# Performance work log

Hardware: AMD Instinct MI355X
Metric: run time of the kernel (lower is better)

Reference implementation:

```python
import jax, jax.numpy as jnp
import numpy as np


def _lstm_last(x, w_ih, w_hh, b_ih, b_hh):
    # x: [M, T, D] -> last hidden state [M, H]; PyTorch gate order i,f,g,o
    M = x.shape[0]
    H = w_hh.shape[1]
    xi = jnp.einsum('mtd,gd->tmg', x, w_ih) + b_ih + b_hh  # [T, M, 4H]
    def step(carry, xt):
        h, c = carry
        gates = xt + h @ w_hh.T
        i, f, g, o = jnp.split(gates, 4, axis=-1)
        c = jax.nn.sigmoid(f) * c + jax.nn.sigmoid(i) * jnp.tanh(g)
        h = jax.nn.sigmoid(o) * jnp.tanh(c)
        return (h, c), None
    z = jnp.zeros((M, H), x.dtype)
    (h, _), _ = jax.lax.scan(step, (z, z), xi)
    return h


def _gcn_conv(x, edge_index, w, b):
    # Symmetric-normalized GCN conv with self loops (PyG GCNConv defaults).
    # x: [BT, N, F] -> [BT, N, Hg]
    N = x.shape[1]
    loops = jnp.arange(N, dtype=edge_index.dtype)
    src = jnp.concatenate([edge_index[0], loops])
    dst = jnp.concatenate([edge_index[1], loops])
    deg = jnp.zeros((N,), x.dtype).at[dst].add(jnp.ones((), x.dtype))
    dinv = jax.lax.rsqrt(deg)  # deg >= 1 thanks to self loops
    norm = (dinv[src] * dinv[dst])[:, None]  # [E+N, 1]
    xw = x @ w                               # [BT, N, Hg]
    msg = xw[:, src, :] * norm               # gather along node axis
    out = jnp.zeros_like(xw).at[:, dst, :].add(msg)  # scatter-add
    return out + b


def setup_inputs() -> dict:
    key = jax.random.key(0)
    ks = jax.random.split(key, 16)
    B, T, N, F = 2, 12, 10000, 16
    Hg, H, P, E = 32, 64, 4, 160000
    sc = 0.1
    return {
        'era5_seq': jax.random.normal(ks[0], (B, T, N, F), jnp.float32),
        'zeta_seq': jax.random.normal(ks[1], (B, T, N), jnp.float32),
        'edge_index': jax.random.randint(ks[2], (2, E), 0, N, jnp.int32),
        'gcn_w': jax.random.normal(ks[3], (F, Hg), jnp.float32) * sc,
        'gcn_b': jnp.zeros((Hg,), jnp.float32),
        'w_ih1': jax.random.normal(ks[4], (4 * H, Hg), jnp.float32) * sc,
        'w_hh1': jax.random.normal(ks[5], (4 * H, H), jnp.float32) * sc,
        'b_ih1': jax.random.normal(ks[6], (4 * H,), jnp.float32) * sc,
        'b_hh1': jax.random.normal(ks[7], (4 * H,), jnp.float32) * sc,
        'w_ih2': jax.random.normal(ks[8], (4 * H, 1), jnp.float32) * sc,
        'w_hh2': jax.random.normal(ks[9], (4 * H, H), jnp.float32) * sc,
        'b_ih2': jax.random.normal(ks[10], (4 * H,), jnp.float32) * sc,
        'b_hh2': jax.random.normal(ks[11], (4 * H,), jnp.float32) * sc,
        'fc_w': jax.random.normal(ks[12], (P, 2 * H), jnp.float32) * sc,
        'fc_b': jnp.zeros((P,), jnp.float32),
    }


def reference(era5_seq, zeta_seq, edge_index, gcn_w, gcn_b, w_ih1, w_hh1, b_ih1, b_hh1, w_ih2, w_hh2, b_ih2, b_hh2, fc_w, fc_b):
    B, T, N, F = era5_seq.shape
    Hg = gcn_w.shape[1]
    # GCN over all (b, t) slices at once (replaces nested python loops)
    h = _gcn_conv(era5_seq.reshape(B * T, N, F), edge_index, gcn_w, gcn_b)
    gcn_seq = h.reshape(B, T, N, Hg).transpose(0, 2, 1, 3).reshape(B * N, T, Hg)
    spatial_feat = _lstm_last(gcn_seq, w_ih1, w_hh1, b_ih1, b_hh1)  # [B*N, H]
    z_seq = zeta_seq.transpose(0, 2, 1).reshape(B * N, T, 1)
    zeta_feat = _lstm_last(z_seq, w_ih2, w_hh2, b_ih2, b_hh2)        # [B*N, H]
    combined = jnp.concatenate([spatial_feat, zeta_feat], axis=-1)
    y = combined @ fc_w.T + fc_b                                     # [B*N, P]
    return y.reshape(B, N, -1).transpose(0, 2, 1)                    # [B, P, N]
```

## Files before the change

kernel.cpp:

```cpp
#include <hip/hip_runtime.h>
#include <hip/hip_bf16.h>
#include <stdint.h>

#define NN 10000
#define EE 160000
#define BB 2
#define TT 12
#define FF 16
#define HG 32
#define HH 64
#define PP 4
#define BT (BB*TT)
#define MM (BB*NN)
#define CAP 96
#define L2E 1.4426950408889634f

typedef _Float16 half8 __attribute__((ext_vector_type(8)));
typedef _Float16 h2 __attribute__((ext_vector_type(2)));
typedef float f32x4 __attribute__((ext_vector_type(4)));

union UP { uint32_t u; h2 h; };
union H8U { uint32_t u[4]; half8 v; };

__device__ __forceinline__ float sigm2(float a) {
  return __builtin_amdgcn_rcpf(1.0f + __builtin_amdgcn_exp2f(-a));
}
__device__ __forceinline__ float tanh2(float a) {
  return fmaf(-2.0f, __builtin_amdgcn_rcpf(1.0f + __builtin_amdgcn_exp2f(a)), 1.0f);
}
__device__ __forceinline__ float tanh2g(float a) {
  return fmaf(-2.0f * (2.0f * L2E),
              __builtin_amdgcn_rcpf(1.0f + __builtin_amdgcn_exp2f(a)),
              2.0f * L2E);
}

__device__ __forceinline__ void barrier_lds() {
  asm volatile("s_waitcnt lgkmcnt(0)" ::: "memory");
  __builtin_amdgcn_s_barrier();
  asm volatile("" ::: "memory");
}

#define FILL_BLKS (EE / 256)
#define PREP_BLKS ((NN * BT * 8) / 256)
__global__ __launch_bounds__(256) void k_prepfill(
    const int* __restrict__ eidx, int* __restrict__ cnt, int* __restrict__ csr,
    const float* __restrict__ era5, uint32_t* __restrict__ xt,
    const float* __restrict__ gcn_w,
    const float* __restrict__ w_ih1, const float* __restrict__ w_hh1,
    const float* __restrict__ b_ih1, const float* __restrict__ b_hh1,
    const float* __restrict__ w_ih2, const float* __restrict__ w_hh2,
    const float* __restrict__ b_ih2, const float* __restrict__ b_hh2,
    uint32_t* __restrict__ wbuf) {
  const int bid = blockIdx.x;
  const int tid = threadIdx.x;
  if (bid < FILL_BLKS) {
    int e = bid * 256 + tid;
    int d = eidx[EE + e];
    int pos = atomicAdd(&cnt[d], 1);
    if (pos < CAP) csr[d * CAP + pos] = eidx[e];
    return;
  }
  if (bid < FILL_BLKS + PREP_BLKS) {
    int D = (bid - FILL_BLKS) * 256 + tid;
    int f2 = D & 7;
    int bt = (D >> 3) % BT;
    int n = D / (8 * BT);
    const float* src = era5 + ((size_t)bt * NN + n) * FF + f2 * 2;
    UP u; u.h[0] = (_Float16)src[0]; u.h[1] = (_Float16)src[1];
    xt[D] = u.u;
    return;
  }
  const int wave = tid >> 6;
  const int lane = tid & 63;
  const int col = lane & 15;
  const int quad = lane >> 4;
#pragma unroll
  for (int g = 0; g < 4; ++g) {
    const float sc = (g == 2) ? 2.0f * L2E : L2E;
    int ncol = 16 * (wave + 4 * g) + col;
    wbuf[(0 + g) * 256 + tid] = __float_as_uint((b_ih1[ncol] + b_hh1[ncol]) * sc);
    wbuf[(4 + g) * 256 + tid] = __float_as_uint((b_ih2[ncol] + b_hh2[ncol]) * sc);
    wbuf[(8 + g) * 256 + tid] = __float_as_uint(w_ih2[ncol] * sc);
    H8U bx;
#pragma unroll
    for (int j = 0; j < 8; ++j)
      bx.v[j] = (_Float16)(w_ih1[ncol * HG + quad * 8 + j] * sc);
#pragma unroll
    for (int d = 0; d < 4; ++d) wbuf[(12 + g * 4 + d) * 256 + tid] = bx.u[d];
#pragma unroll
    for (int c2 = 0; c2 < 2; ++c2) {
      H8U b1, b2;
#pragma unroll
      for (int j = 0; j < 8; ++j) {
        b1.v[j] = (_Float16)(w_hh1[ncol * HH + c2 * 32 + quad * 8 + j] * sc);
        b2.v[j] = (_Float16)(w_hh2[ncol * HH + c2 * 32 + quad * 8 + j] * sc);
      }
#pragma unroll
      for (int d = 0; d < 4; ++d) {
        wbuf[(28 + (g * 2 + c2) * 4 + d) * 256 + tid] = b1.u[d];
        wbuf[(60 + (g * 2 + c2) * 4 + d) * 256 + tid] = b2.u[d];
      }
    }
  }
#pragma unroll
  for (int nt = 0; nt < 2; ++nt) {
#pragma unroll
    for (int d = 0; d < 4; ++d) {
      int k0 = quad * 8 + d * 2;
      int c = nt * 16 + col;
      UP u;
      u.h[0] = (k0 < FF)     ? (_Float16)gcn_w[k0 * HG + c]       : (_Float16)0.f;
      u.h[1] = (k0 + 1 < FF) ? (_Float16)gcn_w[(k0 + 1) * HG + c] : (_Float16)0.f;
      wbuf[(92 + nt * 4 + d) * 256 + tid] = u.u;
    }
  }
}

__global__ __launch_bounds__(256) void k_gather(const uint32_t* __restrict__ xt,
                                                const int* __restrict__ csr,
                                                const int* __restrict__ cnt,
                                                const float* __restrict__ gb,
                                                const uint32_t* __restrict__ wbuf,
                                                _Float16* __restrict__ gout) {
  __shared__ __align__(16) _Float16 aggh[4][32][40];
  const int tid = threadIdx.x;
  const int dloc = tid >> 6, lane = tid & 63;
  const int col = lane & 15, quad = lane >> 4;

  uint32_t* az = (uint32_t*)&aggh[dloc][0][0];
#pragma unroll
  for (int i = 0; i < 10; ++i) az[lane + 64 * i] = 0u;

  H8U Bg[2];
#pragma unroll
  for (int nt = 0; nt < 2; ++nt)
#pragma unroll
    for (int d = 0; d < 4; ++d) Bg[nt].u[d] = wbuf[(92 + nt * 4 + d) * 256 + tid];
  const float b0 = gb[col], b1 = gb[16 + col];

  const int dst = blockIdx.x * 4 + dloc;
  const int cdst = min(cnt[dst], CAP);
  const float dinv_d = rsqrtf((float)cdst + 1.0f);

  float acc[6];
#pragma unroll
  for (int i = 0; i < 6; ++i) acc[i] = 0.f;

  for (int base = 0; base < cdst; base += 64) {
    int mine = base + lane;
    int sv = dst; float dvv = 0.f;
    if (mine < cdst) {
      sv = csr[dst * CAP + mine];
      dvv = rsqrtf((float)cnt[sv] + 1.0f);
    }
    const int lim = min(64, cdst - base);
    for (int j = 0; j < lim; j += 4) {
      int sj[4]; float dj[4];
#pragma unroll
      for (int u = 0; u < 4; ++u) {
        int idx = j + u;
        sj[u] = __shfl(sv, idx);
        float d = __shfl(dvv, idx);
        dj[u] = (idx < lim) ? d : 0.f;
      }
      uint32_t dw[4][3];
#pragma unroll
      for (int u = 0; u < 4; ++u) {
        const uint32_t* row = xt + (size_t)sj[u] * 192;
#pragma unroll
        for (int k = 0; k < 3; ++k) dw[u][k] = row[lane + 64 * k];
      }
#pragma unroll
      for (int u = 0; u < 4; ++u) {
#pragma unroll
        for (int k = 0; k < 3; ++k) {
          UP up; up.u = dw[u][k];
          acc[2 * k]     = fmaf((float)up.h[0], dj[u], acc[2 * k]);
          acc[2 * k + 1] = fmaf((float)up.h[1], dj[u], acc[2 * k + 1]);
        }
      }
    }
  }
  const uint32_t* srow = xt + (size_t)dst * 192;
#pragma unroll
  for (int k = 0; k < 3; ++k) {
    UP u; u.u = srow[lane + 64 * k];
    int d0 = lane + 64 * k;
    int bt = d0 >> 3, f = (d0 & 7) * 2;
    UP o;
    o.h[0] = (_Float16)((acc[2 * k]     + (float)u.h[0] * dinv_d) * dinv_d);
    o.h[1] = (_Float16)((acc[2 * k + 1] + (float)u.h[1] * dinv_d) * dinv_d);
    *(uint32_t*)&aggh[dloc][bt][f] = o.u;
  }
  f32x4 C[2][2];
#pragma unroll
  for (int mt = 0; mt < 2; ++mt) {
    const half8 Af = *(const half8*)&aggh[dloc][mt * 16 + col][quad * 8];
#pragma unroll
    for (int nt = 0; nt < 2; ++nt) {
      float bb = nt ? b1 : b0;
      f32x4 ci; ci[0] = bb; ci[1] = bb; ci[2] = bb; ci[3] = bb;
      C[mt][nt] = __builtin_amdgcn_mfma_f32_16x16x32_f16(Af, Bg[nt].v, ci, 0, 0, 0);
    }
  }
#pragma unroll
  for (int mt = 0; mt < 2; ++mt)
#pragma unroll
    for (int r = 0; r < 4; ++r) {
      int bt = mt * 16 + quad * 4 + r;
      if (bt < BT) {
        int bb = (bt >= TT) ? 1 : 0;
        int t = bt - bb * TT;
#pragma unroll
        for (int nt = 0; nt < 2; ++nt) {
          int c = nt * 16 + col;
          gout[((size_t)(bb * NN + dst)) * 384 + t * 32 + c] = (_Float16)C[mt][nt][r];
        }
      }
    }
}

__global__ __launch_bounds__(256) void k_lstmfc(
    const _Float16* __restrict__ gout, const float* __restrict__ zeta,
    const uint32_t* __restrict__ wbuf,
    const float* __restrict__ fc_w, const float* __restrict__ fc_b,
    float* __restrict__ out) {
  const int m0 = blockIdx.x * 16;
  const int b = (m0 >= NN) ? 1 : 0;
  const int n0 = m0 - b * NN;
  const int tid = threadIdx.x;
  const int wave = tid >> 6;
  const int lane = tid & 63;
  const int col = lane & 15;
  const int quad = lane >> 4;

  float bias1[4], bias2[4], wx[4];
  H8U Bx[4], Bh1[4][2], Bh2[4][2];
#pragma unroll
  for (int g = 0; g < 4; ++g) {
    bias1[g] = __uint_as_float(wbuf[(0 + g) * 256 + tid]);
    bias2[g] = __uint_as_float(wbuf[(4 + g) * 256 + tid]);
    wx[g]    = __uint_as_float(wbuf[(8 + g) * 256 + tid]);
#pragma unroll
    for (int d = 0; d < 4; ++d) Bx[g].u[d] = wbuf[(12 + g * 4 + d) * 256 + tid];
#pragma unroll
    for (int c2 = 0; c2 < 2; ++c2)
#pragma unroll
      for (int d = 0; d < 4; ++d) {
        Bh1[g][c2].u[d] = wbuf[(28 + (g * 2 + c2) * 4 + d) * 256 + tid];
        Bh2[g][c2].u[d] = wbuf[(60 + (g * 2 + c2) * 4 + d) * 256 + tid];
      }
  }
  f32x4 bv1[4];
#pragma unroll
  for (int g = 0; g < 4; ++g) {
    f32x4 v = {bias1[g], bias1[g], bias1[g], bias1[g]};
    bv1[g] = v;
  }

  __shared__ union {
    struct {
      __align__(16) _Float16 hb1[2][16 * 72];
      __align__(16) _Float16 hb2[2][16 * 72];
    } h;
    float fcb[16][132];
  } su;
  __shared__ float zbuf[TT][16];

  if (tid < TT * 16) {
    int t = tid >> 4, s = tid & 15;
    zbuf[t][s] = zeta[((size_t)b * TT + t) * NN + n0 + s];
  }

  const _Float16* gbase = gout + (size_t)(m0 + col) * (TT * HG) + quad * 8;
  half8 A0 = *(const half8*)(gbase);

  float c1[4] = {0.f, 0.f, 0.f, 0.f}, c2v[4] = {0.f, 0.f, 0.f, 0.f};
  float h1f[4], h2f[4];

  barrier_lds();

#pragma unroll
  for (int t = 0; t < TT; ++t) {
    const int p = t & 1;
    if (t > 0) {
#pragma unroll
      for (int r = 0; r < 4; ++r) {
        int a = (quad * 4 + r) * 72 + 16 * wave + col;
        su.h.hb1[p][a] = (_Float16)h1f[r];
        su.h.hb2[p][a] = (_Float16)h2f[r];
      }
    }
    f32x4 a1[4], a2[4];
    const f32x4 z4 = *(const f32x4*)(&zbuf[t][quad * 4]);
#pragma unroll
    for (int g = 0; g < 4; ++g) {
      a1[g] = __builtin_amdgcn_mfma_f32_16x16x32_f16(A0, Bx[g].v, bv1[g], 0, 0, 0);
#pragma unroll
      for (int r = 0; r < 4; ++r)
        a2[g][r] = fmaf(wx[g], z4[r], bias2[g]);
    }
    if (t < TT - 1) A0 = *(const half8*)(gbase + (t + 1) * HG);
    if (t > 0) {
      barrier_lds();
      const half8 A11 = *(const half8*)(&su.h.hb1[p][col * 72 + quad * 8]);
      const half8 A21 = *(const half8*)(&su.h.hb1[p][col * 72 + 32 + quad * 8]);
      const half8 A12 = *(const half8*)(&su.h.hb2[p][col * 72 + quad * 8]);
      const half8 A22 = *(const half8*)(&su.h.hb2[p][col * 72 + 32 + quad * 8]);
#pragma unroll
      for (int g = 0; g < 4; ++g) {
        a1[g] = __builtin_amdgcn_mfma_f32_16x16x32_f16(A11, Bh1[g][0].v, a1[g], 0, 0, 0);
        a1[g] = __builtin_amdgcn_mfma_f32_16x16x32_f16(A21, Bh1[g][1].v, a1[g], 0, 0, 0);
        a2[g] = __builtin_amdgcn_mfma_f32_16x16x32_f16(A12, Bh2[g][0].v, a2[g], 0, 0, 0);
        a2[g] = __builtin_amdgcn_mfma_f32_16x16x32_f16(A22, Bh2[g][1].v, a2[g], 0, 0, 0);
      }
    }
#pragma unroll
    for (int r = 0; r < 4; ++r) {
      float i1 = sigm2(a1[0][r]), f1 = sigm2(a1[1][r]);
      float g1 = tanh2g(a1[2][r]), o1 = sigm2(a1[3][r]);
      c1[r] = fmaf(f1, c1[r], i1 * g1);
      h1f[r] = o1 * tanh2(c1[r]);
      float i2 = sigm2(a2[0][r]), f2 = sigm2(a2[1][r]);
      float g2 = tanh2g(a2[2][r]), o2 = sigm2(a2[3][r]);
      c2v[r] = fmaf(f2, c2v[r], i2 * g2);
      h2f[r] = o2 * tanh2(c2v[r]);
    }
  }
  barrier_lds();
#pragma unroll
  for (int r = 0; r < 4; ++r) {
    su.fcb[quad * 4 + r][16 * wave + col] = h1f[r];
    su.fcb[quad * 4 + r][64 + 16 * wave + col] = h2f[r];
  }
  barrier_lds();
  if (tid < 64) {
    int pp = tid >> 4, s = tid & 15;
    const f32x4* wr = (const f32x4*)(fc_w + pp * 128);
    const float* hv = su.fcb[s];
    float acc = fc_b[pp];
#pragma unroll
    for (int k = 0; k < 32; ++k) {
      f32x4 w4 = wr[k];
      acc += w4[0] * hv[4 * k] + w4[1] * hv[4 * k + 1] +
             w4[2] * hv[4 * k + 2] + w4[3] * hv[4 * k + 3];
    }
    out[((size_t)(b * PP + pp)) * NN + n0 + s] = acc;
  }
}

extern "C" void kernel_launch(void* const* d_in, const int* in_sizes, int n_in,
                              void* d_out, int out_size, void* d_ws, size_t ws_size,
                              hipStream_t stream) {
  (void)in_sizes; (void)n_in; (void)out_size; (void)ws_size;
  const float* era5  = (const float*)d_in[0];
  const float* zeta  = (const float*)d_in[1];
  const int*   eidx  = (const int*)d_in[2];
  const float* gcn_w = (const float*)d_in[3];
  const float* gcn_b = (const float*)d_in[4];
  const float* w_ih1 = (const float*)d_in[5];
  const float* w_hh1 = (const float*)d_in[6];
  const float* b_ih1 = (const float*)d_in[7];
  const float* b_hh1 = (const float*)d_in[8];
  const float* w_ih2 = (const float*)d_in[9];
  const float* w_hh2 = (const float*)d_in[10];
  const float* b_ih2 = (const float*)d_in[11];
  const float* b_hh2 = (const float*)d_in[12];
  const float* fc_w  = (const float*)d_in[13];
  const float* fc_b  = (const float*)d_in[14];
  float* out = (float*)d_out;

  char* ws = (char*)d_ws;
  int*      cnt  = (int*)(ws);
  int*      csr  = (int*)(ws + (64 << 10));
  uint32_t* xt   = (uint32_t*)(ws + (4ull << 20));
  uint32_t* gout = (uint32_t*)(ws + (12ull << 20));
  uint32_t* wbuf = (uint32_t*)(ws + (28ull << 20));

  hipMemsetAsync(cnt, 0, NN * sizeof(int), stream);
  k_prepfill<<<FILL_BLKS + PREP_BLKS + 1, 256, 0, stream>>>(
      eidx, cnt, csr, era5, xt, gcn_w,
      w_ih1, w_hh1, b_ih1, b_hh1, w_ih2, w_hh2, b_ih2, b_hh2, wbuf);
  k_gather<<<NN / 4, 256, 0, stream>>>(xt, csr, cnt, gcn_b, wbuf,
                                       (_Float16*)gout);
  k_lstmfc<<<MM / 16, 256, 0, stream>>>((const _Float16*)gout, zeta, wbuf,
                                        fc_w, fc_b, out);
}
```

Baseline: 176.7 us.

## Slice GCN gather over time chunks and double LSTM rows per block

The prep stage now lays out the fp16 node features as three slices of 8 (batch,time) pairs per node, and the gather kernel launches three times as many blocks, each aggregating one slice with one dword per lane. The aim is to shrink each block's working set for L2 locality and raise parallelism in the gather. The LSTM kernel now runs 512 threads on 32 rows per block, two independent 16-row groups with separate shared buffers, to amortise weight loads and barriers. The cost is that the edge list and degree lookups are re-read once per slice, and the larger blocks raise register and LDS pressure.

```diff
diff --git a/kernel.cpp b/kernel.cpp
--- a/kernel.cpp
+++ b/kernel.cpp
@@ -14,6 +14,8 @@
 #define MM (BB*NN)
 #define CAP 96
 #define L2E 1.4426950408889634f
+#define SL 3
+#define SBT 8
 
 typedef _Float16 half8 __attribute__((ext_vector_type(8)));
 typedef _Float16 h2 __attribute__((ext_vector_type(2)));
@@ -62,10 +64,13 @@
   }
   if (bid < FILL_BLKS + PREP_BLKS) {
     int D = (bid - FILL_BLKS) * 256 + tid;
-    int f2 = D & 7;
-    int bt = (D >> 3) % BT;
-    int n = D / (8 * BT);
-    const float* src = era5 + ((size_t)bt * NN + n) * FF + f2 * 2;
+    int s = D / (NN * 64);
+    int rem = D - s * (NN * 64);
+    int n = rem >> 6;
+    int l = rem & 63;
+    int btl = l >> 3, fp = l & 7;
+    int bt = s * SBT + btl;
+    const float* src = era5 + ((size_t)bt * NN + n) * FF + fp * 2;
     UP u; u.h[0] = (_Float16)src[0]; u.h[1] = (_Float16)src[1];
     xt[D] = u.u;
     return;
@@ -122,14 +127,16 @@
                                                 const float* __restrict__ gb,
                                                 const uint32_t* __restrict__ wbuf,
                                                 _Float16* __restrict__ gout) {
-  __shared__ __align__(16) _Float16 aggh[4][32][40];
+  __shared__ __align__(16) _Float16 aggh[4][16][40];
   const int tid = threadIdx.x;
   const int dloc = tid >> 6, lane = tid & 63;
   const int col = lane & 15, quad = lane >> 4;
+  const int s = blockIdx.x / (NN / 4);
+  const int b2 = blockIdx.x - s * (NN / 4);
 
   uint32_t* az = (uint32_t*)&aggh[dloc][0][0];
 #pragma unroll
-  for (int i = 0; i < 10; ++i) az[lane + 64 * i] = 0u;
+  for (int i = 0; i < 5; ++i) az[lane + 64 * i] = 0u;
 
   H8U Bg[2];
 #pragma unroll
@@ -138,14 +145,12 @@
     for (int d = 0; d < 4; ++d) Bg[nt].u[d] = wbuf[(92 + nt * 4 + d) * 256 + tid];
   const float b0 = gb[col], b1 = gb[16 + col];
 
-  const int dst = blockIdx.x * 4 + dloc;
+  const int dst = b2 * 4 + dloc;
   const int cdst = min(cnt[dst], CAP);
   const float dinv_d = rsqrtf((float)cdst + 1.0f);
-
-  float acc[6];
-#pragma unroll
-  for (int i = 0; i < 6; ++i) acc[i] = 0.f;
-
+  const uint32_t* xs = xt + (size_t)s * NN * 64;
+
+  float a0 = 0.f, a1v = 0.f;
   for (int base = 0; base < cdst; base += 64) {
     int mine = base + lane;
     int sv = dst; float dvv = 0.f;
@@ -154,101 +159,84 @@
       dvv = rsqrtf((float)cnt[sv] + 1.0f);
     }
     const int lim = min(64, cdst - base);
-    for (int j = 0; j < lim; j += 4) {
-      int sj[4]; float dj[4];
-#pragma unroll
-      for (int u = 0; u < 4; ++u) {
+    for (int j = 0; j < lim; j += 8) {
+      int sj[8]; float dj[8];
+#pragma unroll
+      for (int u = 0; u < 8; ++u) {
         int idx = j + u;
         sj[u] = __shfl(sv, idx);
         float d = __shfl(dvv, idx);
         dj[u] = (idx < lim) ? d : 0.f;
       }
-      uint32_t dw[4][3];
-#pragma unroll
-      for (int u = 0; u < 4; ++u) {
-        const uint32_t* row = xt + (size_t)sj[u] * 192;
-#pragma unroll
-        for (int k = 0; k < 3; ++k) dw[u][k] = row[lane + 64 * k];
-      }
-#pragma unroll
-      for (int u = 0; u < 4; ++u) {
-#pragma unroll
-        for (int k = 0; k < 3; ++k) {
-          UP up; up.u = dw[u][k];
-          acc[2 * k]     = fmaf((float)up.h[0], dj[u], acc[2 * k]);
-          acc[2 * k + 1] = fmaf((float)up.h[1], dj[u], acc[2 * k + 1]);
-        }
-      }
-    }
-  }
-  const uint32_t* srow = xt + (size_t)dst * 192;
-#pragma unroll
-  for (int k = 0; k < 3; ++k) {
-    UP u; u.u = srow[lane + 64 * k];
-    int d0 = lane + 64 * k;
-    int bt = d0 >> 3, f = (d0 & 7) * 2;
-    UP o;
-    o.h[0] = (_Float16)((acc[2 * k]     + (float)u.h[0] * dinv_d) * dinv_d);
-    o.h[1] = (_Float16)((acc[2 * k + 1] + (float)u.h[1] * dinv_d) * dinv_d);
-    *(uint32_t*)&aggh[dloc][bt][f] = o.u;
-  }
-  f32x4 C[2][2];
-#pragma unroll
-  for (int mt = 0; mt < 2; ++mt) {
-    const half8 Af = *(const half8*)&aggh[dloc][mt * 16 + col][quad * 8];
-#pragma unroll
-    for (int nt = 0; nt < 2; ++nt) {
-      float bb = nt ? b1 : b0;
-      f32x4 ci; ci[0] = bb; ci[1] = bb; ci[2] = bb; ci[3] = bb;
-      C[mt][nt] = __builtin_amdgcn_mfma_f32_16x16x32_f16(Af, Bg[nt].v, ci, 0, 0, 0);
-    }
-  }
-#pragma unroll
-  for (int mt = 0; mt < 2; ++mt)
+      uint32_t dw[8];
+#pragma unroll
+      for (int u = 0; u < 8; ++u) dw[u] = xs[(size_t)sj[u] * 64 + lane];
+#pragma unroll
+      for (int u = 0; u < 8; ++u) {
+        UP up; up.u = dw[u];
+        a0  = fmaf((float)up.h[0], dj[u], a0);
+        a1v = fmaf((float)up.h[1], dj[u], a1v);
+      }
+    }
+  }
+  UP st; st.u = xs[(size_t)dst * 64 + lane];
+  UP o;
+  o.h[0] = (_Float16)((a0  + (float)st.h[0] * dinv_d) * dinv_d);
+  o.h[1] = (_Float16)((a1v + (float)st.h[1] * dinv_d) * dinv_d);
+  *(uint32_t*)&aggh[dloc][lane >> 3][(lane & 7) * 2] = o.u;
+
+  const half8 Af = *(const half8*)&aggh[dloc][col][quad * 8];
+  f32x4 C[2];
+#pragma unroll
+  for (int nt = 0; nt < 2; ++nt) {
+    float bb = nt ? b1 : b0;
+    f32x4 ci; ci[0] = bb; ci[1] = bb; ci[2] = bb; ci[3] = bb;
+    C[nt] = __builtin_amdgcn_mfma_f32_16x16x32_f16(Af, Bg[nt].v, ci, 0, 0, 0);
+  }
+  if (quad < 2) {
 #pragma unroll
     for (int r = 0; r < 4; ++r) {
-      int bt = mt * 16 + quad * 4 + r;
-      if (bt < BT) {
-        int bb = (bt >= TT) ? 1 : 0;
-        int t = bt - bb * TT;
-#pragma unroll
-        for (int nt = 0; nt < 2; ++nt) {
-          int c = nt * 16 + col;
-          gout[((size_t)(bb * NN + dst)) * 384 + t * 32 + c] = (_Float16)C[mt][nt][r];
-        }
-      }
-    }
-}
-
-__global__ __launch_bounds__(256) void k_lstmfc(
+      int bt = s * SBT + quad * 4 + r;
+      int bb = (bt >= TT) ? 1 : 0;
+      int t = bt - bb * TT;
+#pragma unroll
+      for (int nt = 0; nt < 2; ++nt)
+        gout[((size_t)(bb * NN + dst)) * 384 + t * 32 + nt * 16 + col] =
+            (_Float16)C[nt][r];
+    }
+  }
+}
+
+__global__ __launch_bounds__(512) void k_lstmfc(
     const _Float16* __restrict__ gout, const float* __restrict__ zeta,
     const uint32_t* __restrict__ wbuf,
     const float* __restrict__ fc_w, const float* __restrict__ fc_b,
     float* __restrict__ out) {
-  const int m0 = blockIdx.x * 16;
-  const int b = (m0 >= NN) ? 1 : 0;
-  const int n0 = m0 - b * NN;
+  const int m0 = blockIdx.x * 32;
   const int tid = threadIdx.x;
   const int wave = tid >> 6;
+  const int grp = wave >> 2;
+  const int gw = wave & 3;
   const int lane = tid & 63;
   const int col = lane & 15;
   const int quad = lane >> 4;
+  const int tw = gw * 64 + lane;
 
   float bias1[4], bias2[4], wx[4];
   H8U Bx[4], Bh1[4][2], Bh2[4][2];
 #pragma unroll
   for (int g = 0; g < 4; ++g) {
-    bias1[g] = __uint_as_float(wbuf[(0 + g) * 256 + tid]);
-    bias2[g] = __uint_as_float(wbuf[(4 + g) * 256 + tid]);
-    wx[g]    = __uint_as_float(wbuf[(8 + g) * 256 + tid]);
-#pragma unroll
-    for (int d = 0; d < 4; ++d) Bx[g].u[d] = wbuf[(12 + g * 4 + d) * 256 + tid];
+    bias1[g] = __uint_as_float(wbuf[(0 + g) * 256 + tw]);
+    bias2[g] = __uint_as_float(wbuf[(4 + g) * 256 + tw]);
+    wx[g]    = __uint_as_float(wbuf[(8 + g) * 256 + tw]);
+#pragma unroll
+    for (int d = 0; d < 4; ++d) Bx[g].u[d] = wbuf[(12 + g * 4 + d) * 256 + tw];
 #pragma unroll
     for (int c2 = 0; c2 < 2; ++c2)
 #pragma unroll
       for (int d = 0; d < 4; ++d) {
-        Bh1[g][c2].u[d] = wbuf[(28 + (g * 2 + c2) * 4 + d) * 256 + tid];
-        Bh2[g][c2].u[d] = wbuf[(60 + (g * 2 + c2) * 4 + d) * 256 + tid];
+        Bh1[g][c2].u[d] = wbuf[(28 + (g * 2 + c2) * 4 + d) * 256 + tw];
+        Bh2[g][c2].u[d] = wbuf[(60 + (g * 2 + c2) * 4 + d) * 256 + tw];
       }
   }
   f32x4 bv1[4];
@@ -264,15 +252,19 @@
       __align__(16) _Float16 hb2[2][16 * 72];
     } h;
     float fcb[16][132];
-  } su;
-  __shared__ float zbuf[TT][16];
-
-  if (tid < TT * 16) {
-    int t = tid >> 4, s = tid & 15;
-    zbuf[t][s] = zeta[((size_t)b * TT + t) * NN + n0 + s];
-  }
-
-  const _Float16* gbase = gout + (size_t)(m0 + col) * (TT * HG) + quad * 8;
+  } su[2];
+  __shared__ float zbuf[TT][32];
+
+  if (tid < TT * 32) {
+    int t = tid >> 5, ss = tid & 31;
+    int m = m0 + ss;
+    int bs = (m >= NN) ? 1 : 0;
+    int ns = m - bs * NN;
+    zbuf[t][ss] = zeta[((size_t)bs * TT + t) * NN + ns];
+  }
+
+  const _Float16* gbase =
+      gout + (size_t)(m0 + grp * 16 + col) * (TT * HG) + quad * 8;
   half8 A0 = *(const half8*)(gbase);
 
   float c1[4] = {0.f, 0.f, 0.f, 0.f}, c2v[4] = {0.f, 0.f, 0.f, 0.f};
@@ -286,13 +278,13 @@
     if (t > 0) {
 #pragma unroll
       for (int r = 0; r < 4; ++r) {
-        int a = (quad * 4 + r) * 72 + 16 * wave + col;
-        su.h.hb1[p][a] = (_Float16)h1f[r];
-        su.h.hb2[p][a] = (_Float16)h2f[r];
+        int a = (quad * 4 + r) * 72 + 16 * gw + col;
+        su[grp].h.hb1[p][a] = (_Float16)h1f[r];
+        su[grp].h.hb2[p][a] = (_Float16)h2f[r];
       }
     }
     f32x4 a1[4], a2[4];
-    const f32x4 z4 = *(const f32x4*)(&zbuf[t][quad * 4]);
+    const f32x4 z4 = *(const f32x4*)(&zbuf[t][grp * 16 + quad * 4]);
 #pragma unroll
     for (int g = 0; g < 4; ++g) {
       a1[g] = __builtin_amdgcn_mfma_f32_16x16x32_f16(A0, Bx[g].v, bv1[g], 0, 0, 0);
@@ -303,10 +295,10 @@
     if (t < TT - 1) A0 = *(const half8*)(gbase + (t + 1) * HG);
     if (t > 0) {
       barrier_lds();
-      const half8 A11 = *(const half8*)(&su.h.hb1[p][col * 72 + quad * 8]);
-      const half8 A21 = *(const half8*)(&su.h.hb1[p][col * 72 + 32 + quad * 8]);
-      const half8 A12 = *(const half8*)(&su.h.hb2[p][col * 72 + quad * 8]);
-      const half8 A22 = *(const half8*)(&su.h.hb2[p][col * 72 + 32 + quad * 8]);
+      const half8 A11 = *(const half8*)(&su[grp].h.hb1[p][col * 72 + quad * 8]);
+      const half8 A21 = *(const half8*)(&su[grp].h.hb1[p][col * 72 + 32 + quad * 8]);
+      const half8 A12 = *(const half8*)(&su[grp].h.hb2[p][col * 72 + quad * 8]);
+      const half8 A22 = *(const half8*)(&su[grp].h.hb2[p][col * 72 + 32 + quad * 8]);
 #pragma unroll
       for (int g = 0; g < 4; ++g) {
         a1[g] = __builtin_amdgcn_mfma_f32_16x16x32_f16(A11, Bh1[g][0].v, a1[g], 0, 0, 0);
@@ -330,14 +322,18 @@
   barrier_lds();
 #pragma unroll
   for (int r = 0; r < 4; ++r) {
-    su.fcb[quad * 4 + r][16 * wave + col] = h1f[r];
-    su.fcb[quad * 4 + r][64 + 16 * wave + col] = h2f[r];
+    su[grp].fcb[quad * 4 + r][16 * gw + col] = h1f[r];
+    su[grp].fcb[quad * 4 + r][64 + 16 * gw + col] = h2f[r];
   }
   barrier_lds();
-  if (tid < 64) {
-    int pp = tid >> 4, s = tid & 15;
+  if (tid < 128) {
+    int pp = tid >> 5, ss = tid & 31;
+    int g2 = ss >> 4, sl = ss & 15;
+    int m = m0 + ss;
+    int bs = (m >= NN) ? 1 : 0;
+    int ns = m - bs * NN;
     const f32x4* wr = (const f32x4*)(fc_w + pp * 128);
-    const float* hv = su.fcb[s];
+    const float* hv = su[g2].fcb[sl];
     float acc = fc_b[pp];
 #pragma unroll
     for (int k = 0; k < 32; ++k) {
@@ -345,7 +341,7 @@
       acc += w4[0] * hv[4 * k] + w4[1] * hv[4 * k + 1] +
              w4[2] * hv[4 * k + 2] + w4[3] * hv[4 * k + 3];
     }
-    out[((size_t)(b * PP + pp)) * NN + n0 + s] = acc;
+    out[((size_t)(bs * PP + pp)) * NN + ns] = acc;
   }
 }
 
@@ -381,8 +377,8 @@
   k_prepfill<<<FILL_BLKS + PREP_BLKS + 1, 256, 0, stream>>>(
       eidx, cnt, csr, era5, xt, gcn_w,
       w_ih1, w_hh1, b_ih1, b_hh1, w_ih2, w_hh2, b_ih2, b_hh2, wbuf);
-  k_gather<<<NN / 4, 256, 0, stream>>>(xt, csr, cnt, gcn_b, wbuf,
-                                       (_Float16*)gout);
-  k_lstmfc<<<MM / 16, 256, 0, stream>>>((const _Float16*)gout, zeta, wbuf,
+  k_gather<<<SL * (NN / 4), 256, 0, stream>>>(xt, csr, cnt, gcn_b, wbuf,
+                                              (_Float16*)gout);
+  k_lstmfc<<<MM / 32, 512, 0, stream>>>((const _Float16*)gout, zeta, wbuf,
                                         fc_w, fc_b, out);
 }
```

Result: slower. 187.1 us (+5.9%).

## Fold GCN weight and bias into LSTM input projection, drop GCN matmul

Applied to the files above, without the earlier changes.

Precomputes W_ih1·W_gcn and W_ih1·b_gcn in the weight-prep block, so the LSTM input MFMA consumes the raw 16-feature normalized aggregate directly. The gather kernel no longer runs its MFMA or LDS staging and writes a half-size [M,T,16] intermediate instead of [M,T,32]. The weight-prep block moves to block 0 and stages w_ih1 in 32 KB of LDS, which makes that single block longer. The fused product is rounded to fp16 once rather than twice, which slightly changes numerics.

```diff
diff --git a/kernel.cpp b/kernel.cpp
--- a/kernel.cpp
+++ b/kernel.cpp
@@ -45,7 +45,7 @@
 __global__ __launch_bounds__(256) void k_prepfill(
     const int* __restrict__ eidx, int* __restrict__ cnt, int* __restrict__ csr,
     const float* __restrict__ era5, uint32_t* __restrict__ xt,
-    const float* __restrict__ gcn_w,
+    const float* __restrict__ gcn_w, const float* __restrict__ gcn_b,
     const float* __restrict__ w_ih1, const float* __restrict__ w_hh1,
     const float* __restrict__ b_ih1, const float* __restrict__ b_hh1,
     const float* __restrict__ w_ih2, const float* __restrict__ w_hh2,
@@ -53,15 +53,15 @@
     uint32_t* __restrict__ wbuf) {
   const int bid = blockIdx.x;
   const int tid = threadIdx.x;
-  if (bid < FILL_BLKS) {
-    int e = bid * 256 + tid;
+  if (bid >= 1 && bid <= FILL_BLKS) {
+    int e = (bid - 1) * 256 + tid;
     int d = eidx[EE + e];
     int pos = atomicAdd(&cnt[d], 1);
     if (pos < CAP) csr[d * CAP + pos] = eidx[e];
     return;
   }
-  if (bid < FILL_BLKS + PREP_BLKS) {
-    int D = (bid - FILL_BLKS) * 256 + tid;
+  if (bid > FILL_BLKS) {
+    int D = (bid - 1 - FILL_BLKS) * 256 + tid;
     int f2 = D & 7;
     int bt = (D >> 3) % BT;
     int n = D / (8 * BT);
@@ -70,6 +70,14 @@
     xt[D] = u.u;
     return;
   }
+  __shared__ float wl[256 * HG];
+  __shared__ float gwl[FF * HG];
+  __shared__ float gbl[HG];
+  for (int i = tid; i < 256 * HG; i += 256) wl[i] = w_ih1[i];
+  for (int i = tid; i < FF * HG; i += 256) gwl[i] = gcn_w[i];
+  if (tid < HG) gbl[tid] = gcn_b[tid];
+  __syncthreads();
+
   const int wave = tid >> 6;
   const int lane = tid & 63;
   const int col = lane & 15;
@@ -78,13 +86,22 @@
   for (int g = 0; g < 4; ++g) {
     const float sc = (g == 2) ? 2.0f * L2E : L2E;
     int ncol = 16 * (wave + 4 * g) + col;
-    wbuf[(0 + g) * 256 + tid] = __float_as_uint((b_ih1[ncol] + b_hh1[ncol]) * sc);
+    const float* wr = &wl[ncol * HG];
+    float bc = 0.f;
+    for (int hg = 0; hg < HG; ++hg) bc = fmaf(gbl[hg], wr[hg], bc);
+    wbuf[(0 + g) * 256 + tid] =
+        __float_as_uint((bc + b_ih1[ncol] + b_hh1[ncol]) * sc);
     wbuf[(4 + g) * 256 + tid] = __float_as_uint((b_ih2[ncol] + b_hh2[ncol]) * sc);
     wbuf[(8 + g) * 256 + tid] = __float_as_uint(w_ih2[ncol] * sc);
     H8U bx;
 #pragma unroll
-    for (int j = 0; j < 8; ++j)
-      bx.v[j] = (_Float16)(w_ih1[ncol * HG + quad * 8 + j] * sc);
+    for (int j = 0; j < 8; ++j) {
+      int k = quad * 8 + j;
+      float v = 0.f;
+      if (k < FF)
+        for (int hg = 0; hg < HG; ++hg) v = fmaf(gwl[k * HG + hg], wr[hg], v);
+      bx.v[j] = (_Float16)(v * sc);
+    }
 #pragma unroll
     for (int d = 0; d < 4; ++d) wbuf[(12 + g * 4 + d) * 256 + tid] = bx.u[d];
 #pragma unroll
@@ -102,42 +119,14 @@
       }
     }
   }
-#pragma unroll
-  for (int nt = 0; nt < 2; ++nt) {
-#pragma unroll
-    for (int d = 0; d < 4; ++d) {
-      int k0 = quad * 8 + d * 2;
-      int c = nt * 16 + col;
-      UP u;
-      u.h[0] = (k0 < FF)     ? (_Float16)gcn_w[k0 * HG + c]       : (_Float16)0.f;
-      u.h[1] = (k0 + 1 < FF) ? (_Float16)gcn_w[(k0 + 1) * HG + c] : (_Float16)0.f;
-      wbuf[(92 + nt * 4 + d) * 256 + tid] = u.u;
-    }
-  }
 }
 
 __global__ __launch_bounds__(256) void k_gather(const uint32_t* __restrict__ xt,
                                                 const int* __restrict__ csr,
                                                 const int* __restrict__ cnt,
-                                                const float* __restrict__ gb,
-                                                const uint32_t* __restrict__ wbuf,
-                                                _Float16* __restrict__ gout) {
-  __shared__ __align__(16) _Float16 aggh[4][32][40];
+                                                uint32_t* __restrict__ agg) {
   const int tid = threadIdx.x;
   const int dloc = tid >> 6, lane = tid & 63;
-  const int col = lane & 15, quad = lane >> 4;
-
-  uint32_t* az = (uint32_t*)&aggh[dloc][0][0];
-#pragma unroll
-  for (int i = 0; i < 10; ++i) az[lane + 64 * i] = 0u;
-
-  H8U Bg[2];
-#pragma unroll
-  for (int nt = 0; nt < 2; ++nt)
-#pragma unroll
-    for (int d = 0; d < 4; ++d) Bg[nt].u[d] = wbuf[(92 + nt * 4 + d) * 256 + tid];
-  const float b0 = gb[col], b1 = gb[16 + col];
-
   const int dst = blockIdx.x * 4 + dloc;
   const int cdst = min(cnt[dst], CAP);
   const float dinv_d = rsqrtf((float)cdst + 1.0f);
@@ -186,42 +175,18 @@
   for (int k = 0; k < 3; ++k) {
     UP u; u.u = srow[lane + 64 * k];
     int d0 = lane + 64 * k;
-    int bt = d0 >> 3, f = (d0 & 7) * 2;
+    int bt = d0 >> 3, fp = d0 & 7;
+    int bb = (bt >= TT) ? 1 : 0;
+    int t = bt - bb * TT;
     UP o;
     o.h[0] = (_Float16)((acc[2 * k]     + (float)u.h[0] * dinv_d) * dinv_d);
     o.h[1] = (_Float16)((acc[2 * k + 1] + (float)u.h[1] * dinv_d) * dinv_d);
-    *(uint32_t*)&aggh[dloc][bt][f] = o.u;
-  }
-  f32x4 C[2][2];
-#pragma unroll
-  for (int mt = 0; mt < 2; ++mt) {
-    const half8 Af = *(const half8*)&aggh[dloc][mt * 16 + col][quad * 8];
-#pragma unroll
-    for (int nt = 0; nt < 2; ++nt) {
-      float bb = nt ? b1 : b0;
-      f32x4 ci; ci[0] = bb; ci[1] = bb; ci[2] = bb; ci[3] = bb;
-      C[mt][nt] = __builtin_amdgcn_mfma_f32_16x16x32_f16(Af, Bg[nt].v, ci, 0, 0, 0);
-    }
-  }
-#pragma unroll
-  for (int mt = 0; mt < 2; ++mt)
-#pragma unroll
-    for (int r = 0; r < 4; ++r) {
-      int bt = mt * 16 + quad * 4 + r;
-      if (bt < BT) {
-        int bb = (bt >= TT) ? 1 : 0;
-        int t = bt - bb * TT;
-#pragma unroll
-        for (int nt = 0; nt < 2; ++nt) {
-          int c = nt * 16 + col;
-          gout[((size_t)(bb * NN + dst)) * 384 + t * 32 + c] = (_Float16)C[mt][nt][r];
-        }
-      }
-    }
+    agg[((size_t)(bb * NN + dst) * TT + t) * 8 + fp] = o.u;
+  }
 }
 
 __global__ __launch_bounds__(256) void k_lstmfc(
-    const _Float16* __restrict__ gout, const float* __restrict__ zeta,
+    const _Float16* __restrict__ agg, const float* __restrict__ zeta,
     const uint32_t* __restrict__ wbuf,
     const float* __restrict__ fc_w, const float* __restrict__ fc_b,
     float* __restrict__ out) {
@@ -272,7 +237,8 @@
     zbuf[t][s] = zeta[((size_t)b * TT + t) * NN + n0 + s];
   }
 
-  const _Float16* gbase = gout + (size_t)(m0 + col) * (TT * HG) + quad * 8;
+  const _Float16* gbase =
+      agg + (size_t)(m0 + col) * (TT * FF) + (quad & 1) * 8;
   half8 A0 = *(const half8*)(gbase);
 
   float c1[4] = {0.f, 0.f, 0.f, 0.f}, c2v[4] = {0.f, 0.f, 0.f, 0.f};
@@ -300,7 +266,7 @@
       for (int r = 0; r < 4; ++r)
         a2[g][r] = fmaf(wx[g], z4[r], bias2[g]);
     }
-    if (t < TT - 1) A0 = *(const half8*)(gbase + (t + 1) * HG);
+    if (t < TT - 1) A0 = *(const half8*)(gbase + (t + 1) * FF);
     if (t > 0) {
       barrier_lds();
       const half8 A11 = *(const half8*)(&su.h.hb1[p][col * 72 + quad * 8]);
@@ -374,15 +340,14 @@
   int*      cnt  = (int*)(ws);
   int*      csr  = (int*)(ws + (64 << 10));
   uint32_t* xt   = (uint32_t*)(ws + (4ull << 20));
-  uint32_t* gout = (uint32_t*)(ws + (12ull << 20));
-  uint32_t* wbuf = (uint32_t*)(ws + (28ull << 20));
+  uint32_t* agg  = (uint32_t*)(ws + (12ull << 20));
+  uint32_t* wbuf = (uint32_t*)(ws + (20ull << 20));
 
   hipMemsetAsync(cnt, 0, NN * sizeof(int), stream);
-  k_prepfill<<<FILL_BLKS + PREP_BLKS + 1, 256, 0, stream>>>(
-      eidx, cnt, csr, era5, xt, gcn_w,
+  k_prepfill<<<1 + FILL_BLKS + PREP_BLKS, 256, 0, stream>>>(
+      eidx, cnt, csr, era5, xt, gcn_w, gcn_b,
       w_ih1, w_hh1, b_ih1, b_hh1, w_ih2, w_hh2, b_ih2, b_hh2, wbuf);
-  k_gather<<<NN / 4, 256, 0, stream>>>(xt, csr, cnt, gcn_b, wbuf,
-                                       (_Float16*)gout);
-  k_lstmfc<<<MM / 16, 256, 0, stream>>>((const _Float16*)gout, zeta, wbuf,
+  k_gather<<<NN / 4, 256, 0, stream>>>(xt, csr, cnt, agg);
+  k_lstmfc<<<MM / 16, 256, 0, stream>>>((const _Float16*)agg, zeta, wbuf,
                                         fc_w, fc_b, out);
 }
```

Result: no change. 176.6 us (-0.1%).
